# Kernel optimization log

Measured on AMD Instinct MI355X. Metric: run time of the kernel, lower is better.

## Reference

```python
import jax, jax.numpy as jnp
import numpy as np

N, E, D, K, B = 50000, 600000, 128, 8, 64
E_DIM = 16  # edge_attr feature dim (hard-coded nn.Linear(16, in_dim))


def setup_inputs() -> dict:
    key = jax.random.key(0)
    ks = jax.random.split(key, 10)
    x = jax.random.normal(ks[0], (N, D), dtype=jnp.float32)
    edge_index = jax.random.randint(ks[1], (2, E), 0, N)
    edge_attr = jax.random.normal(ks[2], (E, E_DIM), dtype=jnp.float32)
    # binary pocket membership mask [N, K]
    pkt_mask = (jax.random.uniform(ks[3], (N, K)) < 0.3).astype(jnp.float32)
    batch = jnp.sort(jax.random.randint(ks[4], (N,), 0, B))
    s = 1.0 / np.sqrt(D)
    We = jax.random.normal(ks[5], (E_DIM, D), dtype=jnp.float32) * (1.0 / np.sqrt(E_DIM))
    be = jnp.zeros((D,), jnp.float32)
    W1 = jax.random.normal(ks[6], (D, D), dtype=jnp.float32) * s
    b1 = jnp.zeros((D,), jnp.float32)
    W2 = jax.random.normal(ks[7], (D, D), dtype=jnp.float32) * s
    b2 = jnp.zeros((D,), jnp.float32)
    eps = jnp.zeros((), jnp.float32)  # GINEConv train_eps init 0
    gamma = jnp.ones((D,), jnp.float32)
    beta = jnp.zeros((D,), jnp.float32)
    Wv = jax.random.normal(ks[8], (D, D), dtype=jnp.float32) * s
    bv = jnp.zeros((D,), jnp.float32)
    return {"x": x, "edge_index": edge_index, "edge_attr": edge_attr,
            "pkt_mask": pkt_mask, "batch": batch,
            "We": We, "be": be, "W1": W1, "b1": b1, "W2": W2, "b2": b2,
            "eps": eps, "gamma": gamma, "beta": beta, "Wv": Wv, "bv": bv}


def reference(x, edge_index, edge_attr, pkt_mask, batch,
              We, be, W1, b1, W2, b2, eps, gamma, beta, Wv, bv):
    src, dst = edge_index[0], edge_index[1]
    # edge_lin: [E,16] -> [E,D]
    edge_emb = edge_attr @ We + be
    # GINEConv: message = relu(x_src + edge_emb), scatter-add at dst
    msg = jax.nn.relu(x[src] + edge_emb)
    agg = jax.ops.segment_sum(msg, dst, num_segments=N)
    h = (1.0 + eps) * x + agg
    x_res = jax.nn.relu(h @ W1 + b1) @ W2 + b2  # nn MLP
    # virtual feedback: pocket-wise masked mean pooling per graph
    xw = x_res[:, None, :] * pkt_mask[:, :, None]          # [N,K,D]
    pocket_sum = jax.ops.segment_sum(xw.reshape(N, K * D), batch,
                                     num_segments=B).reshape(B, K, D)
    pocket_count = jax.ops.segment_sum(pkt_mask, batch, num_segments=B)  # [B,K]
    pocket_mean = pocket_sum / (pocket_count[:, :, None] + 1e-9)
    pocket_emb = pocket_mean @ Wv + bv                      # [B,K,D]
    node_pe = pocket_emb[batch]                             # gather -> [N,K,D]
    x_res = x_res + (node_pe * pkt_mask[:, :, None]).sum(axis=1)
    # LayerNorm (eps=1e-5, population variance as in torch)
    mu = x_res.mean(axis=-1, keepdims=True)
    var = ((x_res - mu) ** 2).mean(axis=-1, keepdims=True)
    y = (x_res - mu) / jnp.sqrt(var + 1e-5) * gamma + beta
    # ReLU activation; dropout is identity in eval mode
    return jax.nn.relu(y)
```

## Files before the change

### kernel.cpp

```cpp
#include <hip/hip_runtime.h>
#include <hip/hip_bf16.h>
#include <stdint.h>

#define D 128
#define K 8
#define BGRAPH 64
#define CH 64
#define GRP 4

typedef __attribute__((ext_vector_type(8))) short bf16x8;
typedef __attribute__((ext_vector_type(4))) float f32x4;

__device__ __forceinline__ short f2bf(float f) {
    union { float f; uint32_t u; } v; v.f = f;
    const uint32_t r = (v.u + 0x7fffu + ((v.u >> 16) & 1u)) >> 16;
    return (short)r;
}

__global__ __launch_bounds__(256) void cast_x_kernel(
    const float* __restrict__ x, __hip_bfloat16* __restrict__ xb, int n)
{
    const int i = (blockIdx.x * 256 + threadIdx.x) * 8;
    if (i + 8 > n) return;
    const float4 a = *(const float4*)(x + i);
    const float4 b = *(const float4*)(x + i + 4);
    __hip_bfloat16 v[8];
    v[0] = __float2bfloat16(a.x); v[1] = __float2bfloat16(a.y);
    v[2] = __float2bfloat16(a.z); v[3] = __float2bfloat16(a.w);
    v[4] = __float2bfloat16(b.x); v[5] = __float2bfloat16(b.y);
    v[6] = __float2bfloat16(b.z); v[7] = __float2bfloat16(b.w);
    *(uint4*)(xb + i) = *(const uint4*)v;
}

__global__ __launch_bounds__(128) void cast_w_kernel(
    const float* __restrict__ W1, const float* __restrict__ W2,
    short* __restrict__ wb1t, short* __restrict__ wb2t)
{
    const int which = blockIdx.x >> 7;
    const int n = blockIdx.x & 127;
    const int k = threadIdx.x;
    const float* W = which ? W2 : W1;
    short* O = which ? wb2t : wb1t;
    O[n * D + k] = f2bf(W[(size_t)k * D + n]);
}

__global__ __launch_bounds__(256) void hist_kernel(
    const int* __restrict__ dst, int* __restrict__ deg, int E)
{
    const int i = (blockIdx.x * 256 + threadIdx.x) * 4;
    if (i + 4 <= E) {
        const int4 v = *(const int4*)(dst + i);
        atomicAdd(&deg[v.x], 1);
        atomicAdd(&deg[v.y], 1);
        atomicAdd(&deg[v.z], 1);
        atomicAdd(&deg[v.w], 1);
    } else {
        for (int j = i; j < E; ++j) atomicAdd(&deg[dst[j]], 1);
    }
}

__global__ __launch_bounds__(256) void scan_partial_kernel(
    const int* __restrict__ deg, int* __restrict__ bsum, int N)
{
    const int t = threadIdx.x;
    const int base = (blockIdx.x * 256 + t) * 4;
    int s = 0;
    if (base + 4 <= N) {
        const int4 v = *(const int4*)(deg + base);
        s = v.x + v.y + v.z + v.w;
    } else {
        for (int j = base; j < N; ++j) s += deg[j];
    }
    __shared__ int red[256];
    red[t] = s;
    __syncthreads();
    for (int off = 128; off; off >>= 1) {
        if (t < off) red[t] += red[t + off];
        __syncthreads();
    }
    if (t == 0) bsum[blockIdx.x] = red[0];
}

__global__ __launch_bounds__(64) void scan_top_kernel(
    const int* __restrict__ bsum, int* __restrict__ boffs, int nb)
{
    __shared__ int sh[64];
    const int t = threadIdx.x;
    const int v = (t < nb) ? bsum[t] : 0;
    sh[t] = v;
    __syncthreads();
    for (int off = 1; off < 64; off <<= 1) {
        const int u = (t >= off) ? sh[t - off] : 0;
        __syncthreads();
        sh[t] += u;
        __syncthreads();
    }
    if (t < nb) boffs[t] = sh[t] - v;
}

__global__ __launch_bounds__(256) void scan_final_kernel(
    const int* __restrict__ deg, const int* __restrict__ boffs,
    int* __restrict__ cursor, int N)
{
    const int t = threadIdx.x;
    const int base = (blockIdx.x * 256 + t) * 4;
    int v0 = 0, v1 = 0, v2 = 0, v3 = 0;
    if (base + 4 <= N) {
        const int4 v = *(const int4*)(deg + base);
        v0 = v.x; v1 = v.y; v2 = v.z; v3 = v.w;
    } else {
        if (base     < N) v0 = deg[base];
        if (base + 1 < N) v1 = deg[base + 1];
        if (base + 2 < N) v2 = deg[base + 2];
        if (base + 3 < N) v3 = deg[base + 3];
    }
    const int s = v0 + v1 + v2 + v3;
    __shared__ int sh[256];
    sh[t] = s;
    __syncthreads();
    for (int off = 1; off < 256; off <<= 1) {
        const int u = (t >= off) ? sh[t - off] : 0;
        __syncthreads();
        sh[t] += u;
        __syncthreads();
    }
    int ex = boffs[blockIdx.x] + sh[t] - s;
    if (base < N)     { cursor[base]     = ex; } ex += v0;
    if (base + 1 < N) { cursor[base + 1] = ex; } ex += v1;
    if (base + 2 < N) { cursor[base + 2] = ex; } ex += v2;
    if (base + 3 < N) { cursor[base + 3] = ex; }
}

__global__ __launch_bounds__(256) void scatter_kernel(
    const int* __restrict__ src, const int* __restrict__ dst,
    int* __restrict__ cursor, int4* __restrict__ sde, int E)
{
    const int i = blockIdx.x * 256 + threadIdx.x;
    if (i < E) {
        const int sv = src[i];
        const int dv = dst[i];
        const int p = atomicAdd(&cursor[dv], 1);
        sde[p] = make_int4(sv, dv, i, 0);
    }
}

__device__ __forceinline__ void flush_row(
    float* __restrict__ agg, int node, int d, float2 acc, int first, int last)
{
    float* p = agg + (size_t)node * D + d;
    if (node == first || node == last) {
        if (acc.x != 0.f) atomicAdd(p,     acc.x);
        if (acc.y != 0.f) atomicAdd(p + 1, acc.y);
    } else {
        *(float2*)p = acc;
    }
}

__global__ __launch_bounds__(256) void gine_reduce_kernel(
    const __hip_bfloat16* __restrict__ xb, const int4* __restrict__ sde,
    const float* __restrict__ ea, const float* __restrict__ We,
    const float* __restrict__ be, float* __restrict__ agg, int E)
{
    const int wave = threadIdx.x >> 6;
    const int lane = threadIdx.x & 63;
    const int chunk = __builtin_amdgcn_readfirstlane(blockIdx.x * 4 + wave);
    const int e0 = chunk * CH;
    if (e0 >= E) return;
    const int d = lane * 2;
    const int NG = CH / GRP;

    float2 w[16];
    #pragma unroll
    for (int j = 0; j < 16; ++j) w[j] = *(const float2*)(We + j * D + d);
    const float2 bb = *(const float2*)(be + d);

    int4 mcur[GRP], mnext[GRP];
    #pragma unroll
    for (int j = 0; j < GRP; ++j) mcur[j] = sde[e0 + j];
    #pragma unroll
    for (int j = 0; j < GRP; ++j) mnext[j] = sde[e0 + GRP + j];
    __hip_bfloat162 xcur[GRP];
    #pragma unroll
    for (int j = 0; j < GRP; ++j)
        xcur[j] = *(const __hip_bfloat162*)(xb + (size_t)mcur[j].x * D + d);

    const int first = mcur[0].y;
    const int last  = sde[e0 + CH - 1].y;

    float2 acc = make_float2(0.f, 0.f);
    int cur = first;

    for (int g = 0; g < NG; ++g) {
        int4 mnn[GRP] = {};
        __hip_bfloat162 xn[GRP] = {};
        if (g + 2 < NG) {
            #pragma unroll
            for (int j = 0; j < GRP; ++j) mnn[j] = sde[e0 + (g + 2) * GRP + j];
        }
        if (g + 1 < NG) {
            #pragma unroll
            for (int j = 0; j < GRP; ++j)
                xn[j] = *(const __hip_bfloat162*)(xb + (size_t)mnext[j].x * D + d);
        }

        float4 A[GRP][4];
        #pragma unroll
        for (int j = 0; j < GRP; ++j) {
            const float4* p = (const float4*)(ea + (size_t)mcur[j].z * 16);
            A[j][0] = p[0]; A[j][1] = p[1]; A[j][2] = p[2]; A[j][3] = p[3];
        }

        #pragma unroll
        for (int j = 0; j < GRP; ++j) {
            const int dk = mcur[j].y;
            if (dk != cur) {
                flush_row(agg, cur, d, acc, first, last);
                acc = make_float2(0.f, 0.f);
                cur = dk;
            }
            float m0 = bb.x + __bfloat162float(xcur[j].x);
            float m1 = bb.y + __bfloat162float(xcur[j].y);
            const float av[16] = {
                A[j][0].x, A[j][0].y, A[j][0].z, A[j][0].w,
                A[j][1].x, A[j][1].y, A[j][1].z, A[j][1].w,
                A[j][2].x, A[j][2].y, A[j][2].z, A[j][2].w,
                A[j][3].x, A[j][3].y, A[j][3].z, A[j][3].w};
            #pragma unroll
            for (int jj = 0; jj < 16; ++jj) {
                m0 += av[jj] * w[jj].x;
                m1 += av[jj] * w[jj].y;
            }
            acc.x += m0 > 0.f ? m0 : 0.f;
            acc.y += m1 > 0.f ? m1 : 0.f;
        }

        #pragma unroll
        for (int j = 0; j < GRP; ++j) {
            mcur[j] = mnext[j]; mnext[j] = mnn[j]; xcur[j] = xn[j];
        }
    }
    flush_row(agg, cur, d, acc, first, last);
}

#define MROWS 64
#define HSTR  132
__global__ __launch_bounds__(256) void mlp_mfma_kernel(
    const float* __restrict__ x, const float* __restrict__ agg,
    const float* __restrict__ epsp,
    const short* __restrict__ wb1t, const float* __restrict__ b1,
    const short* __restrict__ wb2t, const float* __restrict__ b2,
    float* __restrict__ xres, int N)
{
    __shared__ float hsh[MROWS * HSTR];
    const int row0 = blockIdx.x * MROWS;
    const float ep = 1.0f + epsp[0];

    for (int i = threadIdx.x; i < MROWS * D / 4; i += 256) {
        const int flat = i * 4;
        const int r = flat >> 7;
        const int c = flat & (D - 1);
        const int row = row0 + r;
        float4 hv = make_float4(0.f, 0.f, 0.f, 0.f);
        if (row < N) {
            const float4 xv = *(const float4*)(x   + (size_t)row * D + c);
            const float4 av = *(const float4*)(agg + (size_t)row * D + c);
            hv = make_float4(ep * xv.x + av.x, ep * xv.y + av.y,
                             ep * xv.z + av.z, ep * xv.w + av.w);
        }
        *(float4*)(hsh + r * HSTR + c) = hv;
    }
    __syncthreads();

    const int lane = threadIdx.x & 63;
    const int wrow = (threadIdx.x >> 6) * 16;
    const int m = lane & 15;
    const int q = lane >> 4;

    f32x4 acc[8];

    #pragma unroll
    for (int ct = 0; ct < 8; ++ct) {
        const float b = b1[ct * 16 + m];
        acc[ct] = (f32x4){b, b, b, b};
    }
    #pragma unroll
    for (int ks = 0; ks < 4; ++ks) {
        const float* ap = hsh + (wrow + m) * HSTR + ks * 32 + q * 8;
        float av[8];
        *(float4*)(av)     = *(const float4*)ap;
        *(float4*)(av + 4) = *(const float4*)(ap + 4);
        bf16x8 a;
        #pragma unroll
        for (int j = 0; j < 8; ++j) a[j] = f2bf(av[j]);
        #pragma unroll
        for (int ct = 0; ct < 8; ++ct) {
            const bf16x8 b = *(const bf16x8*)(wb1t + (ct * 16 + m) * D + ks * 32 + q * 8);
            acc[ct] = __builtin_amdgcn_mfma_f32_16x16x32_bf16(a, b, acc[ct], 0, 0, 0);
        }
    }
    #pragma unroll
    for (int ct = 0; ct < 8; ++ct)
        #pragma unroll
        for (int r = 0; r < 4; ++r) {
            const float v = acc[ct][r];
            hsh[(wrow + q * 4 + r) * HSTR + ct * 16 + m] = v > 0.f ? v : 0.f;
        }

    #pragma unroll
    for (int ct = 0; ct < 8; ++ct) {
        const float b = b2[ct * 16 + m];
        acc[ct] = (f32x4){b, b, b, b};
    }
    #pragma unroll
    for (int ks = 0; ks < 4; ++ks) {
        const float* ap = hsh + (wrow + m) * HSTR + ks * 32 + q * 8;
        float av[8];
        *(float4*)(av)     = *(const float4*)ap;
        *(float4*)(av + 4) = *(const float4*)(ap + 4);
        bf16x8 a;
        #pragma unroll
        for (int j = 0; j < 8; ++j) a[j] = f2bf(av[j]);
        #pragma unroll
        for (int ct = 0; ct < 8; ++ct) {
            const bf16x8 b = *(const bf16x8*)(wb2t + (ct * 16 + m) * D + ks * 32 + q * 8);
            acc[ct] = __builtin_amdgcn_mfma_f32_16x16x32_bf16(a, b, acc[ct], 0, 0, 0);
        }
    }
    #pragma unroll
    for (int r = 0; r < 4; ++r) {
        const int row = row0 + wrow + q * 4 + r;
        if (row < N) {
            #pragma unroll
            for (int ct = 0; ct < 8; ++ct)
                xres[(size_t)row * D + ct * 16 + m] = acc[ct][r];
        }
    }
}

#define PPARTS 32
__global__ __launch_bounds__(128) void pocket_sum_kernel(
    const float* __restrict__ xres, const float* __restrict__ pmask,
    const int* __restrict__ batch,
    float* __restrict__ psum, float* __restrict__ pcnt, int N)
{
    const int g = blockIdx.x / PPARTS;
    const int part = blockIdx.x % PPARTS;

    int lo, hi;
    {
        int l = 0, r = N;
        while (l < r) { int m = (l + r) >> 1; if (batch[m] < g) l = m + 1; else r = m; }
        lo = l;
        r = N;
        while (l < r) { int m = (l + r) >> 1; if (batch[m] < g + 1) l = m + 1; else r = m; }
        hi = l;
    }
    const int cnt = hi - lo;
    const int per = (cnt + PPARTS - 1) / PPARTS;
    const int s = lo + part * per;
    const int e = min(s + per, hi);

    const int d = threadIdx.x;
    float acc[K];
    #pragma unroll
    for (int k = 0; k < K; ++k) acc[k] = 0.0f;
    float c = 0.0f;

    for (int n = s; n < e; ++n) {
        const float xv = xres[(size_t)n * D + d];
        const float4 m0 = *(const float4*)(pmask + (size_t)n * K);
        const float4 m1 = *(const float4*)(pmask + (size_t)n * K + 4);
        acc[0] += m0.x * xv; acc[1] += m0.y * xv;
        acc[2] += m0.z * xv; acc[3] += m0.w * xv;
        acc[4] += m1.x * xv; acc[5] += m1.y * xv;
        acc[6] += m1.z * xv; acc[7] += m1.w * xv;
        if (d < K) c += pmask[(size_t)n * K + d];
    }
    #pragma unroll
    for (int k = 0; k < K; ++k)
        atomicAdd(&psum[(size_t)g * (K * D) + k * D + d], acc[k]);
    if (d < K) atomicAdd(&pcnt[g * K + d], c);
}

__global__ __launch_bounds__(128) void pocket_emb_kernel(
    const float* __restrict__ psum, const float* __restrict__ pcnt,
    const float* __restrict__ Wv, const float* __restrict__ bv,
    float* __restrict__ pemb)
{
    __shared__ float smean[K * D];
    __shared__ float scnt[K];
    const int g = blockIdx.x;
    const int d = threadIdx.x;
    if (d < K) scnt[d] = pcnt[g * K + d];
    __syncthreads();
    #pragma unroll
    for (int k = 0; k < K; ++k)
        smean[k * D + d] = psum[(size_t)g * (K * D) + k * D + d] / (scnt[k] + 1e-9f);
    __syncthreads();

    float acc[K];
    const float bvv = bv[d];
    #pragma unroll
    for (int k = 0; k < K; ++k) acc[k] = bvv;
    for (int j = 0; j < D; ++j) {
        const float w = Wv[j * D + d];
        #pragma unroll
        for (int k = 0; k < K; ++k) acc[k] += smean[k * D + j] * w;
    }
    #pragma unroll
    for (int k = 0; k < K; ++k)
        pemb[(size_t)g * (K * D) + k * D + d] = acc[k];
}

__global__ __launch_bounds__(256) void ln_kernel(
    const float* __restrict__ xres, const float* __restrict__ pmask,
    const int* __restrict__ batch, const float* __restrict__ pemb,
    const float* __restrict__ gamma, const float* __restrict__ beta,
    float* __restrict__ out, int N)
{
    const int wave = threadIdx.x >> 6;
    const int lane = threadIdx.x & 63;
    const int n = blockIdx.x * 4 + wave;
    if (n >= N) return;
    const int d = lane * 2;

    float2 v = *(const float2*)(xres + (size_t)n * D + d);
    const int g = batch[n];
    const float* pe = pemb + (size_t)g * (K * D);
    const float4 m0 = *(const float4*)(pmask + (size_t)n * K);
    const float4 m1 = *(const float4*)(pmask + (size_t)n * K + 4);
    const float mk[K] = {m0.x, m0.y, m0.z, m0.w, m1.x, m1.y, m1.z, m1.w};
    #pragma unroll
    for (int k = 0; k < K; ++k) {
        if (mk[k] != 0.0f) {
            const float2 p = *(const float2*)(pe + k * D + d);
            v.x += mk[k] * p.x;
            v.y += mk[k] * p.y;
        }
    }

    float s = v.x + v.y;
    #pragma unroll
    for (int off = 32; off; off >>= 1) s += __shfl_xor(s, off, 64);
    const float mu = s * (1.0f / 128.0f);
    const float d0 = v.x - mu, d1 = v.y - mu;
    float sq = d0 * d0 + d1 * d1;
    #pragma unroll
    for (int off = 32; off; off >>= 1) sq += __shfl_xor(sq, off, 64);
    const float var = sq * (1.0f / 128.0f);
    const float inv = rsqrtf(var + 1e-5f);

    const float2 gm = *(const float2*)(gamma + d);
    const float2 bt = *(const float2*)(beta + d);
    float y0 = d0 * inv * gm.x + bt.x;
    float y1 = d1 * inv * gm.y + bt.y;
    y0 = y0 > 0.0f ? y0 : 0.0f;
    y1 = y1 > 0.0f ? y1 : 0.0f;
    *(float2*)(out + (size_t)n * D + d) = make_float2(y0, y1);
}

extern "C" void kernel_launch(void* const* d_in, const int* in_sizes, int n_in,
                              void* d_out, int out_size, void* d_ws, size_t ws_size,
                              hipStream_t stream)
{
    const float* x     = (const float*)d_in[0];
    const int*   ei    = (const int*)  d_in[1];
    const float* ea    = (const float*)d_in[2];
    const float* pmask = (const float*)d_in[3];
    const int*   batch = (const int*)  d_in[4];
    const float* We    = (const float*)d_in[5];
    const float* be    = (const float*)d_in[6];
    const float* W1    = (const float*)d_in[7];
    const float* b1    = (const float*)d_in[8];
    const float* W2    = (const float*)d_in[9];
    const float* b2    = (const float*)d_in[10];
    const float* epsp  = (const float*)d_in[11];
    const float* gamma = (const float*)d_in[12];
    const float* beta  = (const float*)d_in[13];
    const float* Wv    = (const float*)d_in[14];
    const float* bv    = (const float*)d_in[15];
    float* out = (float*)d_out;

    const int N = in_sizes[0] / D;
    const int E = in_sizes[1] / 2;
    const int* src = ei;
    const int* dst = ei + E;

    int*   deg  = (int*)d_ws;
    float* agg  = (float*)(deg + N);
    float* psum = agg + (size_t)N * D;
    float* pcnt = psum + (size_t)BGRAPH * K * D;
    float* xres = pcnt + (size_t)BGRAPH * K;
    float* pemb = xres + (size_t)N * D;
    float* extra = pemb + (size_t)BGRAPH * K * D;
    __hip_bfloat16* xb = (__hip_bfloat16*)(extra + 128);
    short* wb1t = (short*)(xb + (size_t)N * D);
    short* wb2t = wb1t + (size_t)D * D;

    int*  cursor = (int*)xres;
    int4* sde    = (int4*)(((uintptr_t)(cursor + N) + 15) & ~(uintptr_t)15);
    int*  bsum   = (int*)extra;
    int*  boffs  = bsum + 64;

    const int nb = (N + 1023) / 1024;
    const int nchunks = (E + CH - 1) / CH;

    const size_t zero_bytes =
        ((size_t)N + (size_t)N * D + (size_t)BGRAPH * K * D + BGRAPH * K) * sizeof(float);
    hipMemsetAsync(d_ws, 0, zero_bytes, stream);

    cast_x_kernel<<<(N * D / 8 + 255) / 256, 256, 0, stream>>>(x, xb, N * D);
    cast_w_kernel<<<256, 128, 0, stream>>>(W1, W2, wb1t, wb2t);
    hist_kernel<<<(E / 4 + 255) / 256, 256, 0, stream>>>(dst, deg, E);
    scan_partial_kernel<<<nb, 256, 0, stream>>>(deg, bsum, N);
    scan_top_kernel<<<1, 64, 0, stream>>>(bsum, boffs, nb);
    scan_final_kernel<<<nb, 256, 0, stream>>>(deg, boffs, cursor, N);
    scatter_kernel<<<(E + 255) / 256, 256, 0, stream>>>(src, dst, cursor, sde, E);
    gine_reduce_kernel<<<(nchunks + 3) / 4, 256, 0, stream>>>(
        xb, sde, ea, We, be, agg, E);

    mlp_mfma_kernel<<<(N + MROWS - 1) / MROWS, 256, 0, stream>>>(
        x, agg, epsp, wb1t, b1, wb2t, b2, xres, N);
    pocket_sum_kernel<<<BGRAPH * PPARTS, 128, 0, stream>>>(
        xres, pmask, batch, psum, pcnt, N);
    pocket_emb_kernel<<<BGRAPH, 128, 0, stream>>>(psum, pcnt, Wv, bv, pemb);
    ln_kernel<<<(N + 3) / 4, 256, 0, stream>>>(
        xres, pmask, batch, pemb, gamma, beta, out, N);
}
```

Baseline: 376.4 us.

## Merge prep kernels, compress edge metadata, and bf16 edge attrs with prefetch

Folds the x cast, weight cast/transpose and degree histogram into one prep kernel, and also casts edge_attr to bf16. Sorted edge metadata shrinks from int4 to uint2 by packing src and dst as 16-bit fields, with the second word holding the edge id. The reduce kernel now prefetches the bf16 edge attributes one group ahead, alongside x. This cuts launches and memory traffic on the gather-heavy path. The costs are an extra full pass over edge_attr, lower precision in the edge embedding, and node ids limited to 65536.

```diff
diff --git a/kernel.cpp b/kernel.cpp
--- a/kernel.cpp
+++ b/kernel.cpp
@@ -16,46 +16,64 @@
     const uint32_t r = (v.u + 0x7fffu + ((v.u >> 16) & 1u)) >> 16;
     return (short)r;
 }
-
-__global__ __launch_bounds__(256) void cast_x_kernel(
-    const float* __restrict__ x, __hip_bfloat16* __restrict__ xb, int n)
-{
-    const int i = (blockIdx.x * 256 + threadIdx.x) * 8;
-    if (i + 8 > n) return;
-    const float4 a = *(const float4*)(x + i);
-    const float4 b = *(const float4*)(x + i + 4);
-    __hip_bfloat16 v[8];
-    v[0] = __float2bfloat16(a.x); v[1] = __float2bfloat16(a.y);
-    v[2] = __float2bfloat16(a.z); v[3] = __float2bfloat16(a.w);
-    v[4] = __float2bfloat16(b.x); v[5] = __float2bfloat16(b.y);
-    v[6] = __float2bfloat16(b.z); v[7] = __float2bfloat16(b.w);
-    *(uint4*)(xb + i) = *(const uint4*)v;
-}
-
-__global__ __launch_bounds__(128) void cast_w_kernel(
+__device__ __forceinline__ float bflo(uint32_t u) {
+    union { uint32_t u; float f; } v; v.u = u << 16; return v.f;
+}
+__device__ __forceinline__ float bfhi(uint32_t u) {
+    union { uint32_t u; float f; } v; v.u = u & 0xffff0000u; return v.f;
+}
+
+__global__ __launch_bounds__(256) void prep_kernel(
+    const float* __restrict__ x, const float* __restrict__ ea,
     const float* __restrict__ W1, const float* __restrict__ W2,
-    short* __restrict__ wb1t, short* __restrict__ wb2t)
-{
-    const int which = blockIdx.x >> 7;
-    const int n = blockIdx.x & 127;
-    const int k = threadIdx.x;
-    const float* W = which ? W2 : W1;
-    short* O = which ? wb2t : wb1t;
-    O[n * D + k] = f2bf(W[(size_t)k * D + n]);
-}
-
-__global__ __launch_bounds__(256) void hist_kernel(
-    const int* __restrict__ dst, int* __restrict__ deg, int E)
-{
-    const int i = (blockIdx.x * 256 + threadIdx.x) * 4;
-    if (i + 4 <= E) {
-        const int4 v = *(const int4*)(dst + i);
-        atomicAdd(&deg[v.x], 1);
-        atomicAdd(&deg[v.y], 1);
-        atomicAdd(&deg[v.z], 1);
-        atomicAdd(&deg[v.w], 1);
+    const int* __restrict__ dst,
+    __hip_bfloat16* __restrict__ xb, short* __restrict__ eab,
+    short* __restrict__ wb1t, short* __restrict__ wb2t,
+    int* __restrict__ deg,
+    int NX, int NEA, int E, int NBX, int NBE, int NBW)
+{
+    const int b = blockIdx.x;
+    const int t = threadIdx.x;
+    if (b < NBX) {
+        const int i = b * 2048 + t * 8;
+        if (i + 8 <= NX) {
+            const float4 a = *(const float4*)(x + i);
+            const float4 c = *(const float4*)(x + i + 4);
+            short v[8];
+            v[0] = f2bf(a.x); v[1] = f2bf(a.y); v[2] = f2bf(a.z); v[3] = f2bf(a.w);
+            v[4] = f2bf(c.x); v[5] = f2bf(c.y); v[6] = f2bf(c.z); v[7] = f2bf(c.w);
+            *(uint4*)((short*)xb + i) = *(const uint4*)v;
+        }
+    } else if (b < NBX + NBE) {
+        const int i = (b - NBX) * 2048 + t * 8;
+        if (i + 8 <= NEA) {
+            const float4 a = *(const float4*)(ea + i);
+            const float4 c = *(const float4*)(ea + i + 4);
+            short v[8];
+            v[0] = f2bf(a.x); v[1] = f2bf(a.y); v[2] = f2bf(a.z); v[3] = f2bf(a.w);
+            v[4] = f2bf(c.x); v[5] = f2bf(c.y); v[6] = f2bf(c.z); v[7] = f2bf(c.w);
+            *(uint4*)(eab + i) = *(const uint4*)v;
+        }
+    } else if (b < NBX + NBE + NBW) {
+        const int idx = (b - NBX - NBE) * 256 + t;
+        const int which = idx >> 14;
+        const int rem = idx & 16383;
+        const int n = rem >> 7;
+        const int k = rem & 127;
+        const float* W = which ? W2 : W1;
+        short* O = which ? wb2t : wb1t;
+        O[n * D + k] = f2bf(W[(size_t)k * D + n]);
     } else {
-        for (int j = i; j < E; ++j) atomicAdd(&deg[dst[j]], 1);
+        const int i = ((b - NBX - NBE - NBW) * 256 + t) * 4;
+        if (i + 4 <= E) {
+            const int4 v = *(const int4*)(dst + i);
+            atomicAdd(&deg[v.x], 1);
+            atomicAdd(&deg[v.y], 1);
+            atomicAdd(&deg[v.z], 1);
+            atomicAdd(&deg[v.w], 1);
+        } else {
+            for (int j = i; j < E; ++j) atomicAdd(&deg[dst[j]], 1);
+        }
     }
 }
 
@@ -133,14 +151,14 @@
 
 __global__ __launch_bounds__(256) void scatter_kernel(
     const int* __restrict__ src, const int* __restrict__ dst,
-    int* __restrict__ cursor, int4* __restrict__ sde, int E)
+    int* __restrict__ cursor, uint2* __restrict__ md, int E)
 {
     const int i = blockIdx.x * 256 + threadIdx.x;
     if (i < E) {
-        const int sv = src[i];
-        const int dv = dst[i];
+        const unsigned sv = (unsigned)src[i];
+        const unsigned dv = (unsigned)dst[i];
         const int p = atomicAdd(&cursor[dv], 1);
-        sde[p] = make_int4(sv, dv, i, 0);
+        md[p] = make_uint2(sv | (dv << 16), (unsigned)i);
     }
 }
 
@@ -157,8 +175,8 @@
 }
 
 __global__ __launch_bounds__(256) void gine_reduce_kernel(
-    const __hip_bfloat16* __restrict__ xb, const int4* __restrict__ sde,
-    const float* __restrict__ ea, const float* __restrict__ We,
+    const __hip_bfloat16* __restrict__ xb, const uint2* __restrict__ md,
+    const short* __restrict__ eab, const float* __restrict__ We,
     const float* __restrict__ be, float* __restrict__ agg, int E)
 {
     const int wave = threadIdx.x >> 6;
@@ -174,45 +192,50 @@
     for (int j = 0; j < 16; ++j) w[j] = *(const float2*)(We + j * D + d);
     const float2 bb = *(const float2*)(be + d);
 
-    int4 mcur[GRP], mnext[GRP];
-    #pragma unroll
-    for (int j = 0; j < GRP; ++j) mcur[j] = sde[e0 + j];
-    #pragma unroll
-    for (int j = 0; j < GRP; ++j) mnext[j] = sde[e0 + GRP + j];
+    uint2 mcur[GRP], mnext[GRP];
+    #pragma unroll
+    for (int j = 0; j < GRP; ++j) mcur[j] = md[e0 + j];
+    #pragma unroll
+    for (int j = 0; j < GRP; ++j) mnext[j] = md[e0 + GRP + j];
+    uint4 eacur[GRP][2];
+    #pragma unroll
+    for (int j = 0; j < GRP; ++j) {
+        const uint4* p = (const uint4*)(eab + (size_t)mcur[j].y * 16);
+        eacur[j][0] = p[0]; eacur[j][1] = p[1];
+    }
     __hip_bfloat162 xcur[GRP];
     #pragma unroll
     for (int j = 0; j < GRP; ++j)
-        xcur[j] = *(const __hip_bfloat162*)(xb + (size_t)mcur[j].x * D + d);
-
-    const int first = mcur[0].y;
-    const int last  = sde[e0 + CH - 1].y;
+        xcur[j] = *(const __hip_bfloat162*)(xb + (size_t)(mcur[j].x & 0xffffu) * D + d);
+
+    const int first = (int)(mcur[0].x >> 16);
+    const int last  = (int)(md[e0 + CH - 1].x >> 16);
 
     float2 acc = make_float2(0.f, 0.f);
     int cur = first;
 
     for (int g = 0; g < NG; ++g) {
-        int4 mnn[GRP] = {};
+        uint2 mnn[GRP] = {};
+        uint4 ean[GRP][2] = {};
         __hip_bfloat162 xn[GRP] = {};
         if (g + 2 < NG) {
             #pragma unroll
-            for (int j = 0; j < GRP; ++j) mnn[j] = sde[e0 + (g + 2) * GRP + j];
+            for (int j = 0; j < GRP; ++j) mnn[j] = md[e0 + (g + 2) * GRP + j];
         }
         if (g + 1 < NG) {
             #pragma unroll
+            for (int j = 0; j < GRP; ++j) {
+                const uint4* p = (const uint4*)(eab + (size_t)mnext[j].y * 16);
+                ean[j][0] = p[0]; ean[j][1] = p[1];
+            }
+            #pragma unroll
             for (int j = 0; j < GRP; ++j)
-                xn[j] = *(const __hip_bfloat162*)(xb + (size_t)mnext[j].x * D + d);
-        }
-
-        float4 A[GRP][4];
+                xn[j] = *(const __hip_bfloat162*)(xb + (size_t)(mnext[j].x & 0xffffu) * D + d);
+        }
+
         #pragma unroll
         for (int j = 0; j < GRP; ++j) {
-            const float4* p = (const float4*)(ea + (size_t)mcur[j].z * 16);
-            A[j][0] = p[0]; A[j][1] = p[1]; A[j][2] = p[2]; A[j][3] = p[3];
-        }
-
-        #pragma unroll
-        for (int j = 0; j < GRP; ++j) {
-            const int dk = mcur[j].y;
+            const int dk = (int)(mcur[j].x >> 16);
             if (dk != cur) {
                 flush_row(agg, cur, d, acc, first, last);
                 acc = make_float2(0.f, 0.f);
@@ -220,11 +243,13 @@
             }
             float m0 = bb.x + __bfloat162float(xcur[j].x);
             float m1 = bb.y + __bfloat162float(xcur[j].y);
+            const uint4 ua = eacur[j][0];
+            const uint4 ub = eacur[j][1];
             const float av[16] = {
-                A[j][0].x, A[j][0].y, A[j][0].z, A[j][0].w,
-                A[j][1].x, A[j][1].y, A[j][1].z, A[j][1].w,
-                A[j][2].x, A[j][2].y, A[j][2].z, A[j][2].w,
-                A[j][3].x, A[j][3].y, A[j][3].z, A[j][3].w};
+                bflo(ua.x), bfhi(ua.x), bflo(ua.y), bfhi(ua.y),
+                bflo(ua.z), bfhi(ua.z), bflo(ua.w), bfhi(ua.w),
+                bflo(ub.x), bfhi(ub.x), bflo(ub.y), bfhi(ub.y),
+                bflo(ub.z), bfhi(ub.z), bflo(ub.w), bfhi(ub.w)};
             #pragma unroll
             for (int jj = 0; jj < 16; ++jj) {
                 m0 += av[jj] * w[jj].x;
@@ -236,7 +261,9 @@
 
         #pragma unroll
         for (int j = 0; j < GRP; ++j) {
-            mcur[j] = mnext[j]; mnext[j] = mnn[j]; xcur[j] = xn[j];
+            mcur[j] = mnext[j]; mnext[j] = mnn[j];
+            eacur[j][0] = ean[j][0]; eacur[j][1] = ean[j][1];
+            xcur[j] = xn[j];
         }
     }
     flush_row(agg, cur, d, acc, first, last);
@@ -497,27 +524,33 @@
     short* wb1t = (short*)(xb + (size_t)N * D);
     short* wb2t = wb1t + (size_t)D * D;
 
-    int*  cursor = (int*)xres;
-    int4* sde    = (int4*)(((uintptr_t)(cursor + N) + 15) & ~(uintptr_t)15);
-    int*  bsum   = (int*)extra;
-    int*  boffs  = bsum + 64;
+    int*   cursor = (int*)xres;
+    uint2* md  = (uint2*)(((uintptr_t)(cursor + N) + 15) & ~(uintptr_t)15);
+    short* eab = (short*)(md + E);
+
+    int*  bsum  = (int*)extra;
+    int*  boffs = bsum + 64;
 
     const int nb = (N + 1023) / 1024;
     const int nchunks = (E + CH - 1) / CH;
+    const int NX = N * D, NEA = E * 16;
+    const int NBX = NX / 2048;
+    const int NBE = (NEA / 8 + 255) / 256;
+    const int NBW = (2 * D * D) / 256;
+    const int NBH = (E / 4 + 255) / 256;
 
     const size_t zero_bytes =
         ((size_t)N + (size_t)N * D + (size_t)BGRAPH * K * D + BGRAPH * K) * sizeof(float);
     hipMemsetAsync(d_ws, 0, zero_bytes, stream);
 
-    cast_x_kernel<<<(N * D / 8 + 255) / 256, 256, 0, stream>>>(x, xb, N * D);
-    cast_w_kernel<<<256, 128, 0, stream>>>(W1, W2, wb1t, wb2t);
-    hist_kernel<<<(E / 4 + 255) / 256, 256, 0, stream>>>(dst, deg, E);
+    prep_kernel<<<NBX + NBE + NBW + NBH, 256, 0, stream>>>(
+        x, ea, W1, W2, dst, xb, eab, wb1t, wb2t, deg, NX, NEA, E, NBX, NBE, NBW);
     scan_partial_kernel<<<nb, 256, 0, stream>>>(deg, bsum, N);
     scan_top_kernel<<<1, 64, 0, stream>>>(bsum, boffs, nb);
     scan_final_kernel<<<nb, 256, 0, stream>>>(deg, boffs, cursor, N);
-    scatter_kernel<<<(E + 255) / 256, 256, 0, stream>>>(src, dst, cursor, sde, E);
+    scatter_kernel<<<(E + 255) / 256, 256, 0, stream>>>(src, dst, cursor, md, E);
     gine_reduce_kernel<<<(nchunks + 3) / 4, 256, 0, stream>>>(
-        xb, sde, ea, We, be, agg, E);
+        xb, md, eab, We, be, agg, E);
 
     mlp_mfma_kernel<<<(N + MROWS - 1) / MROWS, 256, 0, stream>>>(
         x, agg, epsp, wb1t, b1, wb2t, b2, xres, N);
```

Result: faster. 367.7 us (-2.3%).
